# Performance work log

Measured on AMD Instinct MI355X. Metric: run time of the kernel, lower is better.

Reference implementation:

```python
import jax, jax.numpy as jnp
import numpy as np

IN_FEATURES = 1024
OUT_FEATURES = 1024
DEGREE = 8
BATCH = 8192


def setup_inputs() -> dict:
    key = jax.random.key(0)
    kx, kc = jax.random.split(key)
    x = jax.random.normal(kx, (BATCH, IN_FEATURES), dtype=jnp.float32)
    std = 1.0 / (IN_FEATURES * (DEGREE + 1))
    coefficients = std * jax.random.normal(
        kc, (IN_FEATURES, OUT_FEATURES, DEGREE + 1), dtype=jnp.float32)
    return {"x": x, "coefficients": coefficients}


def reference(x, coefficients):
    # x: (B, I); coefficients: (I, O, D+1)
    t = jnp.tanh(x)
    # Chebyshev recursion T_0=1, T_1=t, T_k = 2 t T_{k-1} - T_{k-2}
    vals = [jnp.ones_like(t), t]
    for _ in range(2, DEGREE + 1):
        vals.append(2.0 * t * vals[-1] - vals[-2])
    cheby = jnp.stack(vals, axis=-1)  # (B, I, D+1)
    return jnp.einsum('bid,iod->bo', cheby, coefficients)
```

## Files before the change

### kernel.cpp

```cpp
#include <hip/hip_runtime.h>
#include <hip/hip_bf16.h>
#include <stdint.h>

#define BATCH 8192
#define INF   1024
#define GN    1024
#define GK    8192

typedef __attribute__((ext_vector_type(4))) float floatx4;
typedef __attribute__((ext_vector_type(8))) short short8;

static __device__ __forceinline__ ushort f2bf(float f) {
  union { float f; uint32_t u; } v; v.f = f;
  uint32_t r = v.u + 0x7FFF + ((v.u >> 16) & 1);
  return (ushort)(r >> 16);
}

__global__ __launch_bounds__(256) void repack(const float* __restrict__ coef,
                                              ushort* __restrict__ Wt,
                                              float* __restrict__ bias) {
  __shared__ ushort lds[32 * 9 * 33];
  __shared__ float  bl[32 * 33];
  const int i0 = (blockIdx.x >> 5) << 5;
  const int o0 = (blockIdx.x & 31) << 5;
  const int t = threadIdx.x;
  for (int idx = t; idx < 32 * 288; idx += 256) {
    const int ii  = idx / 288;
    const int rem = idx - ii * 288;
    const float f = coef[(size_t)(i0 + ii) * 9216 + (size_t)o0 * 9 + rem];
    lds[rem * 33 + ii] = f2bf(f);
    const int oo = rem / 9;
    if (rem == oo * 9) bl[oo * 33 + ii] = f;
  }
  __syncthreads();
  if (t < 32) {
    float s = 0.f;
    #pragma unroll
    for (int ii = 0; ii < 32; ++ii) s += bl[t * 33 + ii];
    atomicAdd(&bias[o0 + t], s);
  }
  for (int idx = t; idx < 32 * 8 * 32; idx += 256) {
    const int oo  = idx >> 8;
    const int rem = idx & 255;
    const int d1  = rem >> 5;
    const int ii  = rem & 31;
    Wt[(size_t)(o0 + oo) * GK + (size_t)d1 * 1024 + (i0 + ii)] =
        lds[(oo * 9 + d1 + 1) * 33 + ii];
  }
}

__global__ __launch_bounds__(256) void featurize(const float* __restrict__ x,
                                                 ushort* __restrict__ Cf) {
  const int tid = blockIdx.x * 256 + threadIdx.x;
  const size_t idx4 = (size_t)tid << 2;
  const int b = tid >> 8;
  const int i = (tid & 255) << 2;
  const float4 v = *reinterpret_cast<const float4*>(x + idx4);
  float t[4] = {tanhf(v.x), tanhf(v.y), tanhf(v.z), tanhf(v.w)};
  float Tp[4] = {1.f, 1.f, 1.f, 1.f};
  float Tc[4] = {t[0], t[1], t[2], t[3]};
  ushort* base = Cf + (size_t)b * GK + i;
  #pragma unroll
  for (int d = 1; d <= 8; ++d) {
    ushort4 u;
    u.x = f2bf(Tc[0]); u.y = f2bf(Tc[1]); u.z = f2bf(Tc[2]); u.w = f2bf(Tc[3]);
    *reinterpret_cast<ushort4*>(base + (size_t)(d - 1) * 1024) = u;
    #pragma unroll
    for (int j = 0; j < 4; ++j) {
      const float Tn = 2.f * t[j] * Tc[j] - Tp[j];
      Tp[j] = Tc[j]; Tc[j] = Tn;
    }
  }
}

__global__ __launch_bounds__(256) void gemm_bt(const ushort* __restrict__ A,
                                               const ushort* __restrict__ Bt,
                                               const float* __restrict__ bias,
                                               float* __restrict__ C) {
  __shared__ __align__(16) ushort As[2][128 * 64];
  __shared__ __align__(16) ushort Bs[2][128 * 64];
  const int t = threadIdx.x;
  const int bid = (blockIdx.x & 7) * 64 + (blockIdx.x >> 3);
  const int bm0 = (bid >> 3) << 7;
  const int bn0 = (bid & 7) << 7;
  const int lane = t & 63;
  const int wid = t >> 6;
  const int wm0 = (wid >> 1) << 6;
  const int wn0 = (wid & 1) << 6;
  const int lr = lane & 15;
  const int lk = lane >> 4;

  const int srow = t >> 3;
  const int scol = (((t & 7) ^ (srow & 7)) << 4);
  const char* gA0 = (const char*)(A  + (size_t)(bm0 + srow) * GK) + scol;
  const char* gB0 = (const char*)(Bt + (size_t)(bn0 + srow) * GK) + scol;
  const size_t rstride = (size_t)32 * GK * 2;

  const int rc0 = ((0 + lk) ^ (lr & 7)) << 4;
  const int rc1 = ((4 + lk) ^ (lr & 7)) << 4;

  floatx4 acc[4][4] = {};

#define STAGE(bufi, k0)                                                        \
  do {                                                                         \
    const size_t kb = (size_t)(k0) * 2;                                        \
    _Pragma("unroll")                                                          \
    for (int j = 0; j < 4; ++j) {                                              \
      __builtin_amdgcn_global_load_lds(                                        \
          (const __attribute__((address_space(1))) void*)(gA0 + kb + j * rstride), \
          (__attribute__((address_space(3))) void*)((char*)As[bufi] + j * 4096 + t * 16), \
          16, 0, 0);                                                           \
      __builtin_amdgcn_global_load_lds(                                        \
          (const __attribute__((address_space(1))) void*)(gB0 + kb + j * rstride), \
          (__attribute__((address_space(3))) void*)((char*)Bs[bufi] + j * 4096 + t * 16), \
          16, 0, 0);                                                           \
    }                                                                          \
  } while (0)

  STAGE(0, 0);
  __syncthreads();

  int cur = 0;
  for (int kt = 0; kt < GK / 64; ++kt) {
    if (kt < GK / 64 - 1) {
      if (cur) STAGE(0, (kt + 1) * 64); else STAGE(1, (kt + 1) * 64);
    }
    const char* Ab = (const char*)As[cur];
    const char* Bb = (const char*)Bs[cur];
    short8 af[4][2], bf[4][2];
    #pragma unroll
    for (int mi = 0; mi < 4; ++mi) {
      const int rb = (wm0 + mi * 16 + lr) * 128;
      af[mi][0] = *reinterpret_cast<const short8*>(Ab + rb + rc0);
      af[mi][1] = *reinterpret_cast<const short8*>(Ab + rb + rc1);
    }
    #pragma unroll
    for (int ni = 0; ni < 4; ++ni) {
      const int rb = (wn0 + ni * 16 + lr) * 128;
      bf[ni][0] = *reinterpret_cast<const short8*>(Bb + rb + rc0);
      bf[ni][1] = *reinterpret_cast<const short8*>(Bb + rb + rc1);
    }
    #pragma unroll
    for (int kk = 0; kk < 2; ++kk)
      #pragma unroll
      for (int mi = 0; mi < 4; ++mi)
        #pragma unroll
        for (int ni = 0; ni < 4; ++ni)
          acc[mi][ni] = __builtin_amdgcn_mfma_f32_16x16x32_bf16(af[mi][kk], bf[ni][kk], acc[mi][ni], 0, 0, 0);
    __syncthreads();
    cur ^= 1;
  }
#undef STAGE

  #pragma unroll
  for (int ni = 0; ni < 4; ++ni) {
    const int col = bn0 + wn0 + ni * 16 + lr;
    const float bv = bias[col];
    #pragma unroll
    for (int mi = 0; mi < 4; ++mi) {
      const int row = bm0 + wm0 + mi * 16 + lk * 4;
      #pragma unroll
      for (int r = 0; r < 4; ++r)
        C[(size_t)(row + r) * GN + col] = acc[mi][ni][r] + bv;
    }
  }
}

extern "C" void kernel_launch(void* const* d_in, const int* in_sizes, int n_in,
                              void* d_out, int out_size, void* d_ws, size_t ws_size,
                              hipStream_t stream) {
  const float* x    = (const float*)d_in[0];
  const float* coef = (const float*)d_in[1];
  float* out = (float*)d_out;

  char* ws = (char*)d_ws;
  ushort* Cf   = (ushort*)ws;
  ushort* Wt   = (ushort*)(ws + (size_t)BATCH * GK * 2);
  float*  bias = (float*)(ws + (size_t)BATCH * GK * 2 + (size_t)GN * GK * 2);

  hipMemsetAsync(bias, 0, GN * sizeof(float), stream);
  repack<<<1024, 256, 0, stream>>>(coef, Wt, bias);
  featurize<<<(BATCH * INF / 4) / 256, 256, 0, stream>>>(x, Cf);
  gemm_bt<<<512, 256, 0, stream>>>(Cf, Wt, bias, out);
}
```

Baseline: 274.7 us.

## Restructure GEMM into 256x128 tiles with triple-buffered interleaved load/MFMA pipeline

The GEMM tile grows from 128x128 with 4 waves to 256x128 with 8 waves, and the LDS double buffer becomes a triple buffer in dynamic shared memory. Each k-step is split into four quadrants. Async global-to-LDS loads for the tile two steps ahead are interleaved between MFMA groups, with fine-grained barriers, vmcnt waits and setprio hints. The goal is to hide global load latency and LDS read latency behind MFMA work and cut the per-tile syncthreads stall. In exchange it uses more LDS per block, brings in subtle barrier and vmcnt correctness constraints, and launches only 256 blocks, which may leave compute units underfilled.

```diff
diff --git a/kernel.cpp b/kernel.cpp
--- a/kernel.cpp
+++ b/kernel.cpp
@@ -6,6 +6,15 @@
 #define INF   1024
 #define GN    1024
 #define GK    8192
+
+#define BM 256
+#define BN 128
+#define BK 64
+#define NT (GK / BK)
+#define ABYTES (BM * BK * 2)
+#define BBYTES (BN * BK * 2)
+#define BUFSZ  (ABYTES + BBYTES)
+#define SMEM_BYTES (3 * BUFSZ)
 
 typedef __attribute__((ext_vector_type(4))) float floatx4;
 typedef __attribute__((ext_vector_type(8))) short short8;
@@ -73,84 +82,136 @@
   }
 }
 
-__global__ __launch_bounds__(256) void gemm_bt(const ushort* __restrict__ A,
-                                               const ushort* __restrict__ Bt,
-                                               const float* __restrict__ bias,
-                                               float* __restrict__ C) {
-  __shared__ __align__(16) ushort As[2][128 * 64];
-  __shared__ __align__(16) ushort Bs[2][128 * 64];
+
+__device__ __forceinline__ void gload16(const char* src, char* dstp) {
+  __builtin_amdgcn_global_load_lds(
+      (const __attribute__((address_space(1))) void*)src,
+      (__attribute__((address_space(3))) void*)dstp, 16, 0, 0);
+}
+
+template<int CB, int NB, bool DOSTAGE, bool VM6>
+__device__ __forceinline__ void tile_step(char* smem, int kt,
+    const char* const* gA, const char* const* gB, int dst,
+    int wm0, int wn0, int lr, int lk, floatx4 (&acc)[4][4]) {
+  const char* Ab = smem + CB * BUFSZ;
+  const char* Bb = smem + CB * BUFSZ + ABYTES;
+  const int xm = lr & 7;
+  const size_t kb = (size_t)(kt + 2) * 128;
+  short8 af[4][2], bf[4][2];
+
+#define QUAD(MI0, NI0)                                                         \
+  __builtin_amdgcn_s_setprio(1);                                               \
+  _Pragma("unroll") for (int kk = 0; kk < 2; ++kk)                             \
+    _Pragma("unroll") for (int mi = MI0; mi < MI0 + 2; ++mi)                   \
+      _Pragma("unroll") for (int ni = NI0; ni < NI0 + 2; ++ni)                 \
+        acc[mi][ni] = __builtin_amdgcn_mfma_f32_16x16x32_bf16(                 \
+            af[mi][kk], bf[ni][kk], acc[mi][ni], 0, 0, 0);                     \
+  __builtin_amdgcn_s_setprio(0);
+
+  #pragma unroll
+  for (int mi = 0; mi < 2; ++mi)
+    #pragma unroll
+    for (int kk = 0; kk < 2; ++kk)
+      af[mi][kk] = *reinterpret_cast<const short8*>(
+          Ab + (wm0 + mi * 16 + lr) * 128 + ((((kk << 2) | lk) ^ xm) << 4));
+  #pragma unroll
+  for (int ni = 0; ni < 2; ++ni)
+    #pragma unroll
+    for (int kk = 0; kk < 2; ++kk)
+      bf[ni][kk] = *reinterpret_cast<const short8*>(
+          Bb + (wn0 + ni * 16 + lr) * 128 + ((((kk << 2) | lk) ^ xm) << 4));
+  if (DOSTAGE) {
+    gload16(gA[0] + kb, smem + NB * BUFSZ + 0 * 8192 + dst);
+    gload16(gA[1] + kb, smem + NB * BUFSZ + 1 * 8192 + dst);
+  }
+  __builtin_amdgcn_s_barrier();
+  __builtin_amdgcn_sched_barrier(0);
+  QUAD(0, 0)
+
+  #pragma unroll
+  for (int mi = 2; mi < 4; ++mi)
+    #pragma unroll
+    for (int kk = 0; kk < 2; ++kk)
+      af[mi][kk] = *reinterpret_cast<const short8*>(
+          Ab + (wm0 + mi * 16 + lr) * 128 + ((((kk << 2) | lk) ^ xm) << 4));
+  #pragma unroll
+  for (int ni = 2; ni < 4; ++ni)
+    #pragma unroll
+    for (int kk = 0; kk < 2; ++kk)
+      bf[ni][kk] = *reinterpret_cast<const short8*>(
+          Bb + (wn0 + ni * 16 + lr) * 128 + ((((kk << 2) | lk) ^ xm) << 4));
+  if (DOSTAGE) {
+    gload16(gA[2] + kb, smem + NB * BUFSZ + 2 * 8192 + dst);
+    gload16(gA[3] + kb, smem + NB * BUFSZ + 3 * 8192 + dst);
+  }
+  __builtin_amdgcn_s_barrier();
+  __builtin_amdgcn_sched_barrier(0);
+  QUAD(0, 2)
+
+  if (DOSTAGE) {
+    gload16(gB[0] + kb, smem + NB * BUFSZ + ABYTES + 0 * 8192 + dst);
+    gload16(gB[1] + kb, smem + NB * BUFSZ + ABYTES + 1 * 8192 + dst);
+  }
+  __builtin_amdgcn_s_barrier();
+  __builtin_amdgcn_sched_barrier(0);
+  QUAD(2, 0)
+
+  if (VM6) asm volatile("s_waitcnt vmcnt(6)" ::: "memory");
+  else     asm volatile("s_waitcnt vmcnt(0)" ::: "memory");
+  __builtin_amdgcn_s_barrier();
+  __builtin_amdgcn_sched_barrier(0);
+  QUAD(2, 2)
+#undef QUAD
+}
+
+__global__ __launch_bounds__(512, 2) void gemm_bt(const ushort* __restrict__ A,
+                                                  const ushort* __restrict__ Bt,
+                                                  const float* __restrict__ bias,
+                                                  float* __restrict__ C) {
+  extern __shared__ __align__(16) char smem[];
   const int t = threadIdx.x;
-  const int bid = (blockIdx.x & 7) * 64 + (blockIdx.x >> 3);
-  const int bm0 = (bid >> 3) << 7;
+  const int bid = (blockIdx.x & 7) * 32 + (blockIdx.x >> 3);
+  const int bm0 = (bid >> 3) << 8;
   const int bn0 = (bid & 7) << 7;
   const int lane = t & 63;
-  const int wid = t >> 6;
+  const int wid  = t >> 6;
   const int wm0 = (wid >> 1) << 6;
   const int wn0 = (wid & 1) << 6;
   const int lr = lane & 15;
   const int lk = lane >> 4;
 
   const int srow = t >> 3;
-  const int scol = (((t & 7) ^ (srow & 7)) << 4);
-  const char* gA0 = (const char*)(A  + (size_t)(bm0 + srow) * GK) + scol;
-  const char* gB0 = (const char*)(Bt + (size_t)(bn0 + srow) * GK) + scol;
-  const size_t rstride = (size_t)32 * GK * 2;
-
-  const int rc0 = ((0 + lk) ^ (lr & 7)) << 4;
-  const int rc1 = ((4 + lk) ^ (lr & 7)) << 4;
+  const int schunk = ((t & 7) ^ (srow & 7)) << 4;
+  const char* gA[4]; const char* gB[2];
+  #pragma unroll
+  for (int j = 0; j < 4; ++j)
+    gA[j] = (const char*)(A + (size_t)(bm0 + j * 64 + srow) * GK) + schunk;
+  #pragma unroll
+  for (int j = 0; j < 2; ++j)
+    gB[j] = (const char*)(Bt + (size_t)(bn0 + j * 64 + srow) * GK) + schunk;
+  const int dst = t << 4;
 
   floatx4 acc[4][4] = {};
 
-#define STAGE(bufi, k0)                                                        \
-  do {                                                                         \
-    const size_t kb = (size_t)(k0) * 2;                                        \
-    _Pragma("unroll")                                                          \
-    for (int j = 0; j < 4; ++j) {                                              \
-      __builtin_amdgcn_global_load_lds(                                        \
-          (const __attribute__((address_space(1))) void*)(gA0 + kb + j * rstride), \
-          (__attribute__((address_space(3))) void*)((char*)As[bufi] + j * 4096 + t * 16), \
-          16, 0, 0);                                                           \
-      __builtin_amdgcn_global_load_lds(                                        \
-          (const __attribute__((address_space(1))) void*)(gB0 + kb + j * rstride), \
-          (__attribute__((address_space(3))) void*)((char*)Bs[bufi] + j * 4096 + t * 16), \
-          16, 0, 0);                                                           \
-    }                                                                          \
-  } while (0)
-
-  STAGE(0, 0);
-  __syncthreads();
-
-  int cur = 0;
-  for (int kt = 0; kt < GK / 64; ++kt) {
-    if (kt < GK / 64 - 1) {
-      if (cur) STAGE(0, (kt + 1) * 64); else STAGE(1, (kt + 1) * 64);
-    }
-    const char* Ab = (const char*)As[cur];
-    const char* Bb = (const char*)Bs[cur];
-    short8 af[4][2], bf[4][2];
-    #pragma unroll
-    for (int mi = 0; mi < 4; ++mi) {
-      const int rb = (wm0 + mi * 16 + lr) * 128;
-      af[mi][0] = *reinterpret_cast<const short8*>(Ab + rb + rc0);
-      af[mi][1] = *reinterpret_cast<const short8*>(Ab + rb + rc1);
-    }
-    #pragma unroll
-    for (int ni = 0; ni < 4; ++ni) {
-      const int rb = (wn0 + ni * 16 + lr) * 128;
-      bf[ni][0] = *reinterpret_cast<const short8*>(Bb + rb + rc0);
-      bf[ni][1] = *reinterpret_cast<const short8*>(Bb + rb + rc1);
-    }
-    #pragma unroll
-    for (int kk = 0; kk < 2; ++kk)
-      #pragma unroll
-      for (int mi = 0; mi < 4; ++mi)
-        #pragma unroll
-        for (int ni = 0; ni < 4; ++ni)
-          acc[mi][ni] = __builtin_amdgcn_mfma_f32_16x16x32_bf16(af[mi][kk], bf[ni][kk], acc[mi][ni], 0, 0, 0);
-    __syncthreads();
-    cur ^= 1;
-  }
-#undef STAGE
+  #pragma unroll
+  for (int j = 0; j < 4; ++j) gload16(gA[j], smem + j * 8192 + dst);
+  #pragma unroll
+  for (int j = 0; j < 2; ++j) gload16(gB[j], smem + ABYTES + j * 8192 + dst);
+  #pragma unroll
+  for (int j = 0; j < 4; ++j) gload16(gA[j] + 128, smem + BUFSZ + j * 8192 + dst);
+  #pragma unroll
+  for (int j = 0; j < 2; ++j) gload16(gB[j] + 128, smem + BUFSZ + ABYTES + j * 8192 + dst);
+  asm volatile("s_waitcnt vmcnt(6)" ::: "memory");
+  __builtin_amdgcn_s_barrier();
+  __builtin_amdgcn_sched_barrier(0);
+
+  for (int kt = 0; kt < NT - 2; kt += 3) {
+    tile_step<0, 2, true, true>(smem, kt,     gA, gB, dst, wm0, wn0, lr, lk, acc);
+    tile_step<1, 0, true, true>(smem, kt + 1, gA, gB, dst, wm0, wn0, lr, lk, acc);
+    tile_step<2, 1, true, true>(smem, kt + 2, gA, gB, dst, wm0, wn0, lr, lk, acc);
+  }
+  tile_step<0, 2, false, false>(smem, 126, gA, gB, dst, wm0, wn0, lr, lk, acc);
+  tile_step<1, 0, false, false>(smem, 127, gA, gB, dst, wm0, wn0, lr, lk, acc);
 
   #pragma unroll
   for (int ni = 0; ni < 4; ++ni) {
@@ -178,8 +239,11 @@
   ushort* Wt   = (ushort*)(ws + (size_t)BATCH * GK * 2);
   float*  bias = (float*)(ws + (size_t)BATCH * GK * 2 + (size_t)GN * GK * 2);
 
+  hipFuncSetAttribute(reinterpret_cast<const void*>(&gemm_bt),
+                      hipFuncAttributeMaxDynamicSharedMemorySize, SMEM_BYTES);
+
   hipMemsetAsync(bias, 0, GN * sizeof(float), stream);
   repack<<<1024, 256, 0, stream>>>(coef, Wt, bias);
   featurize<<<(BATCH * INF / 4) / 256, 256, 0, stream>>>(x, Cf);
-  gemm_bt<<<512, 256, 0, stream>>>(Cf, Wt, bias, out);
-}
+  gemm_bt<<<256, 512, SMEM_BYTES, stream>>>(Cf, Wt, bias, out);
+}
```

Measured after the change: 248.7 us. -9.4%, faster.
